# Optimization experiments

Hardware: AMD Instinct MI355X
Metric: run time of the kernel (lower is better)

The kernel has to match this reference:

```python
import jax, jax.numpy as jnp
import numpy as np

B, S, HID, USZ, PSZ, OUT = 128, 512, 768, 200, 200, 200
N_SENT = 16  # 16 sentences of 32 tokens; offsets row = [0,32,...,480,-1]


def setup_inputs() -> dict:
    key = jax.random.key(0)
    ks = jax.random.split(key, 8)
    H = jax.random.normal(ks[0], (B, S, HID), jnp.float32)
    u = jax.random.normal(ks[1], (B, USZ), jnp.float32)
    p = jax.random.normal(ks[2], (B, PSZ), jnp.float32)
    Wh = jax.random.normal(ks[3], (HID, OUT), jnp.float32) * 0.05
    Wu = jax.random.normal(ks[4], (USZ, OUT), jnp.float32) * 0.05
    Wp = jax.random.normal(ks[5], (PSZ, OUT), jnp.float32) * 0.05
    v = jax.random.normal(ks[6], (OUT,), jnp.float32) * 0.05
    b = jnp.zeros((OUT,), jnp.float32)  # torch buffer self.b = zeros
    # offsets: N_SENT sentence starts + trailing -1 sentinel -> [B, N_SENT+1]
    row = jnp.concatenate([jnp.arange(N_SENT, dtype=jnp.int32) * (S // N_SENT),
                           jnp.array([-1], jnp.int32)])
    sentence_offsets = jnp.tile(row[None, :], (B, 1))
    return {"H": H, "u": u, "p": p, "Wh": Wh, "Wu": Wu, "Wp": Wp,
            "v": v, "b": b, "sentence_offsets": sentence_offsets}


def reference(H, u, p, Wh, Wu, Wp, v, b, sentence_offsets):
    # Additive attention scores for every token: v . tanh(Wh H + Wu u + Wp p + b)
    Ht = jnp.einsum('bsh,ho->bso', H, Wh)                      # [B,S,OUT]
    ut = (u @ Wu)[:, None, :]                                  # [B,1,OUT]
    pt = (p @ Wp)[:, None, :]                                  # [B,1,OUT]
    scores = jnp.tanh(Ht + ut + pt + b) @ v                    # [B,S]

    Bsz, Sl, _ = H.shape
    beg = sentence_offsets[:, :-1]                             # [B,M]
    nxt = sentence_offsets[:, 1:]                              # [B,M]
    valid = beg != -1
    # faithful to torch: end = 512 if next==-1 else next-1 (off-by-one kept)
    end = jnp.where(nxt == -1, Sl, nxt - 1)
    t = jnp.arange(Sl)
    mask = valid[:, :, None] & (t[None, None, :] >= beg[:, :, None]) \
           & (t[None, None, :] < end[:, :, None])              # [B,M,S]

    neg_inf = jnp.float32(-jnp.inf)
    em = jnp.where(mask, scores[:, None, :], neg_inf)
    m = jnp.max(em, axis=-1, keepdims=True)
    w = jnp.exp(em - jnp.where(jnp.isfinite(m), m, 0.0)) * mask
    denom = jnp.sum(w, axis=-1, keepdims=True)
    alphas = w / jnp.where(denom > 0, denom, 1.0)              # ragged softmax
    # per-sentence weighted sum of H -> [B, M, HID] (invalid sentences = 0)
    return jnp.einsum('bms,bsh->bmh', alphas, H)
```

## Files before the change

kernel.cpp:

```cpp
#include <hip/hip_runtime.h>
#include <hip/hip_bf16.h>
#include <math.h>

#define Bn   128
#define Sn   512
#define HIDn 768
#define OUTn 200
#define MSEG 16
#define NPAD 208
#define NT   13
#define KIT  (HIDn / 32)

typedef __attribute__((ext_vector_type(8))) short short8;
typedef __attribute__((ext_vector_type(4))) float f32x4;

static __device__ inline unsigned short f2bf(float f) {
  union { float f; unsigned u; } v; v.f = f;
  unsigned r = v.u + 0x7FFFu + ((v.u >> 16) & 1u);
  return (unsigned short)(r >> 16);
}

static __device__ inline float fast_tanh(float x) {
  float t = fabsf(x);
  float e = __expf(-2.f * t);
  float r = (1.f - e) * __builtin_amdgcn_rcpf(1.f + e);
  return copysignf(r, x);
}

__global__ __launch_bounds__(256) void setup_kernel(
    const float* __restrict__ Wh, const float* __restrict__ v,
    unsigned short* __restrict__ WhF, float* __restrict__ vP) {
  int idx = blockIdx.x * 256 + threadIdx.x;
  if (blockIdx.x == 0 && threadIdx.x < NPAD)
    vP[threadIdx.x] = (threadIdx.x < OUTn) ? v[threadIdx.x] : 0.f;
  if (idx < NPAD * HIDn) {
    int n = idx / HIDn;
    int k = idx - n * HIDn;
    float val = (n < OUTn) ? Wh[(size_t)k * OUTn + n] : 0.f;
    size_t d = ((size_t)(k >> 5) * NT + (n >> 4)) * 512
             + ((k >> 3) & 3) * 128 + (n & 15) * 8 + (k & 7);
    WhF[d] = f2bf(val);
  }
}

__global__ __launch_bounds__(256) void bias_kernel(
    const float* __restrict__ u, const float* __restrict__ p,
    const float* __restrict__ Wu, const float* __restrict__ Wp,
    const float* __restrict__ bvec, float* __restrict__ biasP) {
  int b = blockIdx.x;
  __shared__ float ul[OUTn], pl[OUTn];
  int tid = threadIdx.x;
  if (tid < OUTn) { ul[tid] = u[b * OUTn + tid]; pl[tid] = p[b * OUTn + tid]; }
  __syncthreads();
  if (tid < NPAD) {
    float s0 = 0.f, s1 = 0.f;
    if (tid < OUTn) {
      s0 = bvec[tid];
      for (int k = 0; k < OUTn; k += 2) {
        s0 += ul[k] * Wu[k * OUTn + tid] + pl[k] * Wp[k * OUTn + tid];
        s1 += ul[k + 1] * Wu[(k + 1) * OUTn + tid] + pl[k + 1] * Wp[(k + 1) * OUTn + tid];
      }
    }
    biasP[(size_t)b * NPAD + tid] = s0 + s1;
  }
}

__global__ __launch_bounds__(256, 2) void fused_kernel(
    const float* __restrict__ H, const unsigned short* __restrict__ WhF,
    const float* __restrict__ biasP, const float* __restrict__ vP,
    const int* __restrict__ offs, float* __restrict__ out) {
  __shared__ float al[128];
  int tid = threadIdx.x, wave = tid >> 6, lane = tid & 63;
  int quad = lane >> 4, l16 = lane & 15;
  int m0 = blockIdx.x * 128;
  int b = m0 >> 9;
  int s0 = m0 & 511;

  f32x4 acc[2][NT];
  for (int mt = 0; mt < 2; ++mt)
    for (int nt = 0; nt < NT; ++nt) acc[mt][nt] = (f32x4){0.f, 0.f, 0.f, 0.f};

  const float* Abase = H + (size_t)(m0 + wave * 32 + l16) * HIDn + quad * 8;
  const short8* Bw = (const short8*)WhF + lane;

  float4 f[2][2][2];
#pragma unroll
  for (int mt = 0; mt < 2; ++mt) {
    const float* ap = Abase + (size_t)mt * 16 * HIDn;
    f[0][mt][0] = *(const float4*)ap;
    f[0][mt][1] = *(const float4*)(ap + 4);
  }

#pragma unroll
  for (int it = 0; it < KIT; ++it) {
    int cur = it & 1;
    if (it + 1 < KIT) {
#pragma unroll
      for (int mt = 0; mt < 2; ++mt) {
        const float* ap = Abase + (size_t)mt * 16 * HIDn + (it + 1) * 32;
        f[1 - cur][mt][0] = *(const float4*)ap;
        f[1 - cur][mt][1] = *(const float4*)(ap + 4);
      }
    }
    short8 bfr[NT];
#pragma unroll
    for (int nt = 0; nt < NT; ++nt)
      bfr[nt] = Bw[(it * NT + nt) * 64];

    short8 a[2];
#pragma unroll
    for (int mt = 0; mt < 2; ++mt) {
      short8 t;
      t[0] = f2bf(f[cur][mt][0].x); t[1] = f2bf(f[cur][mt][0].y);
      t[2] = f2bf(f[cur][mt][0].z); t[3] = f2bf(f[cur][mt][0].w);
      t[4] = f2bf(f[cur][mt][1].x); t[5] = f2bf(f[cur][mt][1].y);
      t[6] = f2bf(f[cur][mt][1].z); t[7] = f2bf(f[cur][mt][1].w);
      a[mt] = t;
    }
#pragma unroll
    for (int nt = 0; nt < NT; ++nt) {
      acc[0][nt] = __builtin_amdgcn_mfma_f32_16x16x32_bf16(a[0], bfr[nt], acc[0][nt], 0, 0, 0);
      acc[1][nt] = __builtin_amdgcn_mfma_f32_16x16x32_bf16(a[1], bfr[nt], acc[1][nt], 0, 0, 0);
    }
  }

  const float* bp = biasP + (size_t)b * NPAD;
  float sc[2][4];
#pragma unroll
  for (int mt = 0; mt < 2; ++mt) {
#pragma unroll
    for (int r = 0; r < 4; ++r) {
      float s = 0.f;
#pragma unroll
      for (int nt = 0; nt < NT; ++nt) {
        int n = nt * 16 + l16;
        s += fast_tanh(acc[mt][nt][r] + bp[n]) * vP[n];
      }
      s += __shfl_xor(s, 1); s += __shfl_xor(s, 2);
      s += __shfl_xor(s, 4); s += __shfl_xor(s, 8);
      sc[mt][r] = s;
    }
  }

  int seg = (s0 >> 5) + wave;
  int beg = offs[b * (MSEG + 1) + seg];
  int nxt = offs[b * (MSEG + 1) + seg + 1];
  bool valid = (beg != -1);
  int end = (nxt == -1) ? Sn : nxt - 1;

  float x[2][4];
  float mx = -INFINITY;
#pragma unroll
  for (int mt = 0; mt < 2; ++mt)
#pragma unroll
    for (int r = 0; r < 4; ++r) {
      int row = s0 + wave * 32 + mt * 16 + quad * 4 + r;
      bool in = valid && row >= beg && row < end;
      x[mt][r] = in ? sc[mt][r] : -INFINITY;
      mx = fmaxf(mx, x[mt][r]);
    }
  mx = fmaxf(mx, __shfl_xor(mx, 16));
  mx = fmaxf(mx, __shfl_xor(mx, 32));
  float mm = (mx > -1e30f) ? mx : 0.f;

  float e[2][4], ls = 0.f;
#pragma unroll
  for (int mt = 0; mt < 2; ++mt)
#pragma unroll
    for (int r = 0; r < 4; ++r) {
      e[mt][r] = __expf(x[mt][r] - mm);
      ls += e[mt][r];
    }
  ls += __shfl_xor(ls, 16);
  ls += __shfl_xor(ls, 32);
  float inv = (ls > 0.f) ? 1.f / ls : 0.f;

  if (l16 == 0) {
#pragma unroll
    for (int mt = 0; mt < 2; ++mt)
#pragma unroll
      for (int r = 0; r < 4; ++r)
        al[wave * 32 + mt * 16 + quad * 4 + r] = e[mt][r] * inv;
  }

  const float4* Hrow = (const float4*)(H + (size_t)(b * Sn + s0 + wave * 32) * HIDn);
  float4 o0 = {0,0,0,0}, o1 = {0,0,0,0}, o2 = {0,0,0,0};
  for (int i = 0; i < 32; ++i) {
    float a = al[wave * 32 + i];
    if (a != 0.f) {
      const float4* hp = Hrow + (size_t)i * (HIDn / 4);
      float4 h0 = hp[lane], h1 = hp[lane + 64], h2 = hp[lane + 128];
      o0.x += a * h0.x; o0.y += a * h0.y; o0.z += a * h0.z; o0.w += a * h0.w;
      o1.x += a * h1.x; o1.y += a * h1.y; o1.z += a * h1.z; o1.w += a * h1.w;
      o2.x += a * h2.x; o2.y += a * h2.y; o2.z += a * h2.z; o2.w += a * h2.w;
    }
  }
  float4* op = (float4*)(out + ((size_t)b * MSEG + seg) * HIDn);
  op[lane] = o0; op[lane + 64] = o1; op[lane + 128] = o2;
}

extern "C" void kernel_launch(void* const* d_in, const int* in_sizes, int n_in,
                              void* d_out, int out_size, void* d_ws, size_t ws_size,
                              hipStream_t stream) {
  const float* H    = (const float*)d_in[0];
  const float* u    = (const float*)d_in[1];
  const float* p    = (const float*)d_in[2];
  const float* Wh   = (const float*)d_in[3];
  const float* Wu   = (const float*)d_in[4];
  const float* Wp   = (const float*)d_in[5];
  const float* v    = (const float*)d_in[6];
  const float* bvec = (const float*)d_in[7];
  const int*   offs = (const int*)d_in[8];
  float* out = (float*)d_out;

  float* biasP = (float*)d_ws;
  float* vP    = biasP + (size_t)Bn * NPAD;
  unsigned short* WhF = (unsigned short*)(vP + NPAD);

  setup_kernel<<<(NPAD * HIDn + 255) / 256, 256, 0, stream>>>(Wh, v, WhF, vP);
  bias_kernel<<<Bn, 256, 0, stream>>>(u, p, Wu, Wp, bvec, biasP);
  fused_kernel<<<(Bn * Sn) / 128, 256, 0, stream>>>(H, WhF, biasP, vP, offs, out);
}
```

Measured before the change: 361.6 us.

## Assign one sentence per block, split N across waves with cross-wave score reduction

Each block now handles one 32-token sentence instead of 128 rows. Its four waves split the GEMM as 2 M-halves by 2 N-halves, with 7 N tiles each after padding N to 224, and the B fragments are double-buffered alongside the A prefetch. Partial scores are combined through shared memory, and each wave accumulates the weighted sum over 8 rows before a shared-memory reduction. The grid is four times larger, with fewer accumulators per wave and higher occupancy, at the cost of extra barriers, a padded tile of wasted MFMA work, and reading each WhF tile more times.

```diff
diff --git a/kernel.cpp b/kernel.cpp
--- a/kernel.cpp
+++ b/kernel.cpp
@@ -1,5 +1,4 @@
 #include <hip/hip_runtime.h>
-#include <hip/hip_bf16.h>
 #include <math.h>
 
 #define Bn   128
@@ -7,8 +6,9 @@
 #define HIDn 768
 #define OUTn 200
 #define MSEG 16
-#define NPAD 208
-#define NT   13
+#define NPAD 224
+#define NT   14
+#define NTW  7
 #define KIT  (HIDn / 32)
 
 typedef __attribute__((ext_vector_type(8))) short short8;
@@ -65,138 +65,133 @@
   }
 }
 
-__global__ __launch_bounds__(256, 2) void fused_kernel(
+__global__ __launch_bounds__(256, 4) void fused_kernel(
     const float* __restrict__ H, const unsigned short* __restrict__ WhF,
     const float* __restrict__ biasP, const float* __restrict__ vP,
     const int* __restrict__ offs, float* __restrict__ out) {
-  __shared__ float al[128];
+  __shared__ float scp[2][32];
+  __shared__ float o_l[4][HIDn];
+
   int tid = threadIdx.x, wave = tid >> 6, lane = tid & 63;
   int quad = lane >> 4, l16 = lane & 15;
-  int m0 = blockIdx.x * 128;
-  int b = m0 >> 9;
-  int s0 = m0 & 511;
-
-  f32x4 acc[2][NT];
-  for (int mt = 0; mt < 2; ++mt)
-    for (int nt = 0; nt < NT; ++nt) acc[mt][nt] = (f32x4){0.f, 0.f, 0.f, 0.f};
-
-  const float* Abase = H + (size_t)(m0 + wave * 32 + l16) * HIDn + quad * 8;
+  int mh = wave >> 1, nh = wave & 1;
+  int bid = blockIdx.x;
+  int b = bid >> 4, seg = bid & 15;
+  int s0 = seg << 5;
+
+  f32x4 acc[NTW];
+#pragma unroll
+  for (int j = 0; j < NTW; ++j) acc[j] = (f32x4){0.f, 0.f, 0.f, 0.f};
+
+  const float* Abase = H + (size_t)(b * Sn + s0 + mh * 16 + l16) * HIDn + quad * 8;
   const short8* Bw = (const short8*)WhF + lane;
 
-  float4 f[2][2][2];
-#pragma unroll
-  for (int mt = 0; mt < 2; ++mt) {
-    const float* ap = Abase + (size_t)mt * 16 * HIDn;
-    f[0][mt][0] = *(const float4*)ap;
-    f[0][mt][1] = *(const float4*)(ap + 4);
-  }
+  float4 f[2][2];
+  short8 bfr[2][NTW];
+  f[0][0] = *(const float4*)Abase;
+  f[0][1] = *(const float4*)(Abase + 4);
+#pragma unroll
+  for (int j = 0; j < NTW; ++j)
+    bfr[0][j] = Bw[(nh * NTW + j) * 64];
 
 #pragma unroll
   for (int it = 0; it < KIT; ++it) {
     int cur = it & 1;
     if (it + 1 < KIT) {
-#pragma unroll
-      for (int mt = 0; mt < 2; ++mt) {
-        const float* ap = Abase + (size_t)mt * 16 * HIDn + (it + 1) * 32;
-        f[1 - cur][mt][0] = *(const float4*)ap;
-        f[1 - cur][mt][1] = *(const float4*)(ap + 4);
-      }
+      const float* ap = Abase + (it + 1) * 32;
+      f[1 - cur][0] = *(const float4*)ap;
+      f[1 - cur][1] = *(const float4*)(ap + 4);
+#pragma unroll
+      for (int j = 0; j < NTW; ++j)
+        bfr[1 - cur][j] = Bw[((it + 1) * NT + nh * NTW + j) * 64];
     }
-    short8 bfr[NT];
-#pragma unroll
-    for (int nt = 0; nt < NT; ++nt)
-      bfr[nt] = Bw[(it * NT + nt) * 64];
-
-    short8 a[2];
-#pragma unroll
-    for (int mt = 0; mt < 2; ++mt) {
-      short8 t;
-      t[0] = f2bf(f[cur][mt][0].x); t[1] = f2bf(f[cur][mt][0].y);
-      t[2] = f2bf(f[cur][mt][0].z); t[3] = f2bf(f[cur][mt][0].w);
-      t[4] = f2bf(f[cur][mt][1].x); t[5] = f2bf(f[cur][mt][1].y);
-      t[6] = f2bf(f[cur][mt][1].z); t[7] = f2bf(f[cur][mt][1].w);
-      a[mt] = t;
-    }
-#pragma unroll
-    for (int nt = 0; nt < NT; ++nt) {
-      acc[0][nt] = __builtin_amdgcn_mfma_f32_16x16x32_bf16(a[0], bfr[nt], acc[0][nt], 0, 0, 0);
-      acc[1][nt] = __builtin_amdgcn_mfma_f32_16x16x32_bf16(a[1], bfr[nt], acc[1][nt], 0, 0, 0);
-    }
-  }
-
-  const float* bp = biasP + (size_t)b * NPAD;
-  float sc[2][4];
-#pragma unroll
-  for (int mt = 0; mt < 2; ++mt) {
+    short8 a;
+    a[0] = f2bf(f[cur][0].x); a[1] = f2bf(f[cur][0].y);
+    a[2] = f2bf(f[cur][0].z); a[3] = f2bf(f[cur][0].w);
+    a[4] = f2bf(f[cur][1].x); a[5] = f2bf(f[cur][1].y);
+    a[6] = f2bf(f[cur][1].z); a[7] = f2bf(f[cur][1].w);
+#pragma unroll
+    for (int j = 0; j < NTW; ++j)
+      acc[j] = __builtin_amdgcn_mfma_f32_16x16x32_bf16(a, bfr[cur][j], acc[j], 0, 0, 0);
+  }
+
+  {
+    const float* bp = biasP + (size_t)b * NPAD + nh * (NTW * 16) + l16;
+    const float* vp = vP + nh * (NTW * 16) + l16;
+    float bv[NTW], vv[NTW];
+#pragma unroll
+    for (int j = 0; j < NTW; ++j) { bv[j] = bp[j * 16]; vv[j] = vp[j * 16]; }
 #pragma unroll
     for (int r = 0; r < 4; ++r) {
       float s = 0.f;
 #pragma unroll
-      for (int nt = 0; nt < NT; ++nt) {
-        int n = nt * 16 + l16;
-        s += fast_tanh(acc[mt][nt][r] + bp[n]) * vP[n];
-      }
+      for (int j = 0; j < NTW; ++j)
+        s += fast_tanh(acc[j][r] + bv[j]) * vv[j];
       s += __shfl_xor(s, 1); s += __shfl_xor(s, 2);
       s += __shfl_xor(s, 4); s += __shfl_xor(s, 8);
-      sc[mt][r] = s;
+      if (l16 == 0) scp[nh][mh * 16 + quad * 4 + r] = s;
     }
   }
-
-  int seg = (s0 >> 5) + wave;
+  __syncthreads();
+
   int beg = offs[b * (MSEG + 1) + seg];
   int nxt = offs[b * (MSEG + 1) + seg + 1];
   bool valid = (beg != -1);
   int end = (nxt == -1) ? Sn : nxt - 1;
 
-  float x[2][4];
-  float mx = -INFINITY;
-#pragma unroll
-  for (int mt = 0; mt < 2; ++mt)
-#pragma unroll
-    for (int r = 0; r < 4; ++r) {
-      int row = s0 + wave * 32 + mt * 16 + quad * 4 + r;
-      bool in = valid && row >= beg && row < end;
-      x[mt][r] = in ? sc[mt][r] : -INFINITY;
-      mx = fmaxf(mx, x[mt][r]);
-    }
-  mx = fmaxf(mx, __shfl_xor(mx, 16));
-  mx = fmaxf(mx, __shfl_xor(mx, 32));
+  float x = -INFINITY;
+  if (lane < 32) {
+    int row = s0 + lane;
+    if (valid && row >= beg && row < end)
+      x = scp[0][lane] + scp[1][lane];
+  }
+  float mx = x;
+  mx = fmaxf(mx, __shfl_xor(mx, 1));  mx = fmaxf(mx, __shfl_xor(mx, 2));
+  mx = fmaxf(mx, __shfl_xor(mx, 4));  mx = fmaxf(mx, __shfl_xor(mx, 8));
+  mx = fmaxf(mx, __shfl_xor(mx, 16)); mx = fmaxf(mx, __shfl_xor(mx, 32));
   float mm = (mx > -1e30f) ? mx : 0.f;
-
-  float e[2][4], ls = 0.f;
-#pragma unroll
-  for (int mt = 0; mt < 2; ++mt)
-#pragma unroll
-    for (int r = 0; r < 4; ++r) {
-      e[mt][r] = __expf(x[mt][r] - mm);
-      ls += e[mt][r];
-    }
-  ls += __shfl_xor(ls, 16);
-  ls += __shfl_xor(ls, 32);
+  float e = __expf(x - mm);
+  float ls = e;
+  ls += __shfl_xor(ls, 1);  ls += __shfl_xor(ls, 2);
+  ls += __shfl_xor(ls, 4);  ls += __shfl_xor(ls, 8);
+  ls += __shfl_xor(ls, 16); ls += __shfl_xor(ls, 32);
   float inv = (ls > 0.f) ? 1.f / ls : 0.f;
-
-  if (l16 == 0) {
-#pragma unroll
-    for (int mt = 0; mt < 2; ++mt)
-#pragma unroll
-      for (int r = 0; r < 4; ++r)
-        al[wave * 32 + mt * 16 + quad * 4 + r] = e[mt][r] * inv;
-  }
-
-  const float4* Hrow = (const float4*)(H + (size_t)(b * Sn + s0 + wave * 32) * HIDn);
+  float av = e * inv;
+
+  float af[8];
+#pragma unroll
+  for (int i = 0; i < 8; ++i) af[i] = __shfl(av, wave * 8 + i);
+
+  const float4* Hrow = (const float4*)(H + (size_t)(b * Sn + s0 + wave * 8) * HIDn);
   float4 o0 = {0,0,0,0}, o1 = {0,0,0,0}, o2 = {0,0,0,0};
-  for (int i = 0; i < 32; ++i) {
-    float a = al[wave * 32 + i];
-    if (a != 0.f) {
-      const float4* hp = Hrow + (size_t)i * (HIDn / 4);
-      float4 h0 = hp[lane], h1 = hp[lane + 64], h2 = hp[lane + 128];
-      o0.x += a * h0.x; o0.y += a * h0.y; o0.z += a * h0.z; o0.w += a * h0.w;
-      o1.x += a * h1.x; o1.y += a * h1.y; o1.z += a * h1.z; o1.w += a * h1.w;
-      o2.x += a * h2.x; o2.y += a * h2.y; o2.z += a * h2.z; o2.w += a * h2.w;
-    }
-  }
-  float4* op = (float4*)(out + ((size_t)b * MSEG + seg) * HIDn);
-  op[lane] = o0; op[lane + 64] = o1; op[lane + 128] = o2;
+#pragma unroll
+  for (int i = 0; i < 8; ++i) {
+    const float4* hp = Hrow + (size_t)i * (HIDn / 4);
+    float4 h0 = hp[lane], h1 = hp[lane + 64], h2 = hp[lane + 128];
+    float a = af[i];
+    o0.x += a * h0.x; o0.y += a * h0.y; o0.z += a * h0.z; o0.w += a * h0.w;
+    o1.x += a * h1.x; o1.y += a * h1.y; o1.z += a * h1.z; o1.w += a * h1.w;
+    o2.x += a * h2.x; o2.y += a * h2.y; o2.z += a * h2.z; o2.w += a * h2.w;
+  }
+  {
+    float4* ol = (float4*)o_l[wave];
+    ol[lane] = o0; ol[lane + 64] = o1; ol[lane + 128] = o2;
+  }
+  __syncthreads();
+
+  if (tid < 192) {
+    const float4* p0 = (const float4*)o_l[0];
+    const float4* p1 = (const float4*)o_l[1];
+    const float4* p2 = (const float4*)o_l[2];
+    const float4* p3 = (const float4*)o_l[3];
+    float4 a0 = p0[tid], a1 = p1[tid], a2 = p2[tid], a3 = p3[tid];
+    float4 s;
+    s.x = a0.x + a1.x + a2.x + a3.x;
+    s.y = a0.y + a1.y + a2.y + a3.y;
+    s.z = a0.z + a1.z + a2.z + a3.z;
+    s.w = a0.w + a1.w + a2.w + a3.w;
+    ((float4*)(out + ((size_t)b * MSEG + seg) * HIDn))[tid] = s;
+  }
 }
 
 extern "C" void kernel_launch(void* const* d_in, const int* in_sizes, int n_in,
@@ -219,5 +214,5 @@
 
   setup_kernel<<<(NPAD * HIDn + 255) / 256, 256, 0, stream>>>(Wh, v, WhF, vP);
   bias_kernel<<<Bn, 256, 0, stream>>>(u, p, Wu, Wp, bvec, biasP);
-  fused_kernel<<<(Bn * Sn) / 128, 256, 0, stream>>>(H, WhF, biasP, vP, offs, out);
-}
+  fused_kernel<<<(Bn * Sn) / 32, 256, 0, stream>>>(H, WhF, biasP, vP, offs, out);
+}
```

After: 403.6 us. 1.12x slower.
